# Kernel optimization log

Measured on AMD Instinct MI355X. Metric: run time of the kernel, lower is better.

## Reference

```python
import jax, jax.numpy as jnp
import numpy as np

N, E, F_IN, H, F_OUT = 50000, 400000, 128, 256, 1
EPS = 1e-5


def setup_inputs() -> dict:
    key = jax.random.key(0)
    ks = jax.random.split(key, 10)
    s = lambda fan_in: 1.0 / np.sqrt(fan_in)
    return {
        "x": jax.random.normal(ks[0], (N, F_IN), dtype=jnp.float32),
        "edge_index": jax.random.randint(ks[1], (2, E), 0, N, dtype=jnp.int64),
        # gcn1: GCNConv(F_IN -> H) + BatchNorm1d(H) params
        "W1": jax.random.uniform(ks[2], (F_IN, H), jnp.float32, -s(F_IN), s(F_IN)),
        "b1": jnp.zeros((H,), jnp.float32),
        "gamma": jnp.ones((H,), jnp.float32),
        "beta": jnp.zeros((H,), jnp.float32),
        # gcn2: GCNConv(H -> H)
        "W2": jax.random.uniform(ks[3], (H, H), jnp.float32, -s(H), s(H)),
        "b2": jnp.zeros((H,), jnp.float32),
        # ClassifierMLP2(2H -> F_OUT): Linear(2H, H) -> ReLU -> Linear(H, F_OUT)
        "Wm1": jax.random.uniform(ks[4], (2 * H, H), jnp.float32, -s(2 * H), s(2 * H)),
        "bm1": jnp.zeros((H,), jnp.float32),
        "Wm2": jax.random.uniform(ks[5], (H, F_OUT), jnp.float32, -s(H), s(H)),
        "bm2": jnp.zeros((F_OUT,), jnp.float32),
    }


def _gcn_conv(x, W, b, src_full, dst_full, norm):
    # x' = D^{-1/2} (A + I) D^{-1/2} X W + b   (self loops already appended)
    xw = x @ W                                  # [N, H]
    msg = xw[src_full] * norm[:, None]          # [E+N, H] gather + scale
    agg = jax.ops.segment_sum(msg, dst_full, num_segments=N)  # scatter-add
    return agg + b


def reference(x, edge_index, W1, b1, gamma, beta, W2, b2, Wm1, bm1, Wm2, bm2):
    src, dst = edge_index[0], edge_index[1]
    loop = jnp.arange(N, dtype=edge_index.dtype)
    src_full = jnp.concatenate([src, loop])     # add_self_loops
    dst_full = jnp.concatenate([dst, loop])
    deg = jax.ops.segment_sum(jnp.ones_like(dst_full, dtype=x.dtype), dst_full,
                              num_segments=N)   # degree of A + I (>= 1)
    dinv = jax.lax.rsqrt(deg)
    norm = dinv[src_full] * dinv[dst_full]      # [E+N] symmetric norm

    # gcn1: conv -> batchnorm (batch stats) -> relu
    h = _gcn_conv(x, W1, b1, src_full, dst_full, norm)
    mu = jnp.mean(h, axis=0)
    var = jnp.mean(jnp.square(h - mu), axis=0)  # biased var, as in BN forward
    h = (h - mu) * jax.lax.rsqrt(var + EPS) * gamma + beta
    h = jax.nn.relu(h)

    # gcn2: conv -> relu
    h = jax.nn.relu(_gcn_conv(h, W2, b2, src_full, dst_full, norm))

    # mix_node_features 'cat': per-edge concat of endpoint features
    edges_x = jnp.concatenate([h[src], h[dst]], axis=-1)  # [E, 2H]

    # ClassifierMLP2 + sigmoid
    out = jax.nn.relu(edges_x @ Wm1 + bm1) @ Wm2 + bm2
    return jax.nn.sigmoid(out)                  # [E, 1]
```

## Files before the change

### kernel.cpp

```cpp
#include <hip/hip_runtime.h>
#include <math.h>

#define NN 50000
#define EE 400000
#define FIN 128
#define HH 256
#define BN_EPS 1e-5f

typedef __attribute__((ext_vector_type(8))) short short8v;
typedef __attribute__((ext_vector_type(4))) short short4v;
typedef __attribute__((ext_vector_type(2))) short short2v;
typedef __attribute__((ext_vector_type(4))) float f32x4;

__device__ inline short f2bf(float x) {
    union { float f; unsigned u; } c; c.f = x;
    unsigned r = c.u + 0x7FFF + ((c.u >> 16) & 1);
    return (short)(r >> 16);
}
__device__ inline float bf2f(short b) {
    union { unsigned u; float f; } c; c.u = ((unsigned)(unsigned short)b) << 16;
    return c.f;
}


__global__ void k_count(const int* __restrict__ dst, int* __restrict__ cnt) {
    int e = blockIdx.x * 256 + threadIdx.x;
    if (e < EE) atomicAdd(&cnt[dst[e]], 1);
}

__global__ void k_dinv(const int* __restrict__ cnt, float* __restrict__ dinv) {
    int n = blockIdx.x * 256 + threadIdx.x;
    if (n < NN) dinv[n] = rsqrtf((float)(cnt[n] + 1));
}

__global__ __launch_bounds__(1024) void k_scan(const int* __restrict__ cnt,
                                               int* __restrict__ row_start,
                                               int* __restrict__ cursor) {
    __shared__ int sums[1024];
    int tid = threadIdx.x;
    const int per = (NN + 1023) / 1024;
    int beg = tid * per;
    int end = min(beg + per, NN);
    int s = 0;
    for (int i = beg; i < end; ++i) s += cnt[i];
    sums[tid] = s;
    __syncthreads();
    for (int off = 1; off < 1024; off <<= 1) {
        int v = (tid >= off) ? sums[tid - off] : 0;
        __syncthreads();
        if (tid >= off) sums[tid] += v;
        __syncthreads();
    }
    int prefix = (tid == 0) ? 0 : sums[tid - 1];
    for (int i = beg; i < end; ++i) {
        row_start[i] = prefix;
        cursor[i] = prefix;
        prefix += cnt[i];
    }
    if (tid == 0) row_start[NN] = sums[1023];
}

__global__ void k_fill(const int* __restrict__ src, const int* __restrict__ dst,
                       int* __restrict__ cursor, int* __restrict__ csr_src) {
    int e = blockIdx.x * 256 + threadIdx.x;
    if (e < EE) {
        int pos = atomicAdd(&cursor[dst[e]], 1);
        csr_src[pos] = src[e];
    }
}


__global__ void k_scaleX(const float* __restrict__ x, const float* __restrict__ dinv,
                         float* __restrict__ Xs) {
    int i4 = blockIdx.x * 256 + threadIdx.x;
    if (i4 >= NN * FIN / 4) return;
    float g = dinv[i4 >> 5];
    float4 v = reinterpret_cast<const float4*>(x)[i4];
    v.x *= g; v.y *= g; v.z *= g; v.w *= g;
    reinterpret_cast<float4*>(Xs)[i4] = v;
}

__global__ void k_wsplit(const float* __restrict__ src, short* __restrict__ hi,
                         short* __restrict__ lo, int K, int NC) {
    int i = blockIdx.x * 256 + threadIdx.x;
    if (i >= K * NC) return;
    int k = i / NC, n = i - k * NC;
    float v = src[i];
    short h = f2bf(v);
    short lw = f2bf(v - bf2f(h));
    size_t d = ((size_t)(k >> 3) * NC + n) * 8 + (k & 7);
    hi[d] = h;
    lo[d] = lw;
}

__global__ void k_wsplit_cat(const float* __restrict__ Wm1, short* __restrict__ hi,
                             short* __restrict__ lo) {
    int i = blockIdx.x * 256 + threadIdx.x;
    if (i >= 256 * 512) return;
    int k = i >> 9, c = i & 511;
    float v = (c < 256) ? Wm1[k * 256 + c] : Wm1[(256 + k) * 256 + (c - 256)];
    short h = f2bf(v);
    short lw = f2bf(v - bf2f(h));
    size_t d = ((size_t)(k >> 3) * 512 + c) * 8 + (k & 7);
    hi[d] = h;
    lo[d] = lw;
}


__global__ __launch_bounds__(256) void k_aggX(const float* __restrict__ Xs,
                                              const int* __restrict__ csr_src,
                                              const int* __restrict__ row_start,
                                              const float* __restrict__ dinv,
                                              short* __restrict__ Ghi,
                                              short* __restrict__ Glo) {
    int wave = threadIdx.x >> 6, lane = threadIdx.x & 63;
    int n = blockIdx.x * 4 + wave;
    if (n >= NN) return;
    const float2* base = reinterpret_cast<const float2*>(Xs);
    float2 v = base[(size_t)n * 64 + lane];
    int s0 = row_start[n], s1 = row_start[n + 1];
    for (int j = s0; j < s1; ++j) {
        float2 u = base[(size_t)csr_src[j] * 64 + lane];
        v.x += u.x; v.y += u.y;
    }
    float g = dinv[n];
    v.x *= g; v.y *= g;
    short2v h, lw;
    short h0 = f2bf(v.x), h1 = f2bf(v.y);
    h[0] = h0; h[1] = h1;
    lw[0] = f2bf(v.x - bf2f(h0)); lw[1] = f2bf(v.y - bf2f(h1));
    *(short2v*)(Ghi + (size_t)n * FIN + lane * 2) = h;
    *(short2v*)(Glo + (size_t)n * FIN + lane * 2) = lw;
}

__global__ __launch_bounds__(256) void k_aggH(const float* __restrict__ T,
                                              const int* __restrict__ csr_src,
                                              const int* __restrict__ row_start,
                                              const float* __restrict__ dinv,
                                              short* __restrict__ Ghi,
                                              short* __restrict__ Glo) {
    int wave = threadIdx.x >> 6, lane = threadIdx.x & 63;
    int n = blockIdx.x * 4 + wave;
    if (n >= NN) return;
    const float4* base = reinterpret_cast<const float4*>(T);
    float4 v = base[(size_t)n * 64 + lane];
    int s0 = row_start[n], s1 = row_start[n + 1];
    for (int j = s0; j < s1; ++j) {
        float4 u = base[(size_t)csr_src[j] * 64 + lane];
        v.x += u.x; v.y += u.y; v.z += u.z; v.w += u.w;
    }
    float g = dinv[n];
    float o[4] = {v.x * g, v.y * g, v.z * g, v.w * g};
    short4v h, lw;
#pragma unroll
    for (int j = 0; j < 4; ++j) {
        short hh = f2bf(o[j]);
        h[j] = hh;
        lw[j] = f2bf(o[j] - bf2f(hh));
    }
    *(short4v*)(Ghi + (size_t)n * HH + lane * 4) = h;
    *(short4v*)(Glo + (size_t)n * HH + lane * 4) = lw;
}


template<int K, int NC, int EPI>
__global__ __launch_bounds__(256, 2) void gemm_stripe(
    const short* __restrict__ Ahi, const short* __restrict__ Alo,
    const short* __restrict__ Bthi, const short* __restrict__ Btlo,
    const float* __restrict__ bias,
    float* __restrict__ OutF, short* __restrict__ OutH, short* __restrict__ OutL,
    short* __restrict__ OutA, short* __restrict__ OutB2, int M)
{
    constexpr int NKT = K / 32;
    constexpr int NSLAB = K / 8;
    constexpr int NPASS = NC / 64;
    __shared__ short lds[2 * NSLAB * 512];
    const int tid = threadIdx.x;
    const int w = tid >> 6, l = tid & 63;
    const int wr = w >> 1, wc = w & 1;
    const int m0 = blockIdx.x * 64;
    const int lhi = l >> 4, llo = l & 15;

    for (int s = w; s < 2 * NSLAB; s += 4) {
        int kg = (s < NSLAB) ? s : (s - NSLAB);
        const short* srcp = (s < NSLAB) ? Ahi : Alo;
        int row = m0 + l;
        if (row > M - 1) row = M - 1;
        short8v v = *(const short8v*)(srcp + (size_t)row * K + kg * 8);
        *(short8v*)(&lds[s * 512 + l * 8]) = v;
    }
    __syncthreads();

    for (int pass = 0; pass < NPASS; ++pass) {
        const int n0 = pass * 64 + wc * 32;
        f32x4 acc[2][2] = {};
#pragma unroll
        for (int kt = 0; kt < NKT; ++kt) {
            short8v bh[2], bl[2];
#pragma unroll
            for (int nt = 0; nt < 2; ++nt) {
                size_t idx = ((size_t)(kt * 4 + lhi) * NC + (n0 + nt * 16 + llo)) * 8;
                bh[nt] = *(const short8v*)(Bthi + idx);
                bl[nt] = *(const short8v*)(Btlo + idx);
            }
            short8v ah[2], al[2];
#pragma unroll
            for (int mt = 0; mt < 2; ++mt) {
                int off = (kt * 4 + lhi) * 512 + (wr * 32 + mt * 16 + llo) * 8;
                ah[mt] = *(const short8v*)(&lds[off]);
                al[mt] = *(const short8v*)(&lds[off + NSLAB * 512]);
            }
#pragma unroll
            for (int mt = 0; mt < 2; ++mt)
#pragma unroll
                for (int nt = 0; nt < 2; ++nt) {
                    acc[mt][nt] = __builtin_amdgcn_mfma_f32_16x16x32_bf16(ah[mt], bh[nt], acc[mt][nt], 0, 0, 0);
                    acc[mt][nt] = __builtin_amdgcn_mfma_f32_16x16x32_bf16(ah[mt], bl[nt], acc[mt][nt], 0, 0, 0);
                    acc[mt][nt] = __builtin_amdgcn_mfma_f32_16x16x32_bf16(al[mt], bh[nt], acc[mt][nt], 0, 0, 0);
                }
        }
#pragma unroll
        for (int mt = 0; mt < 2; ++mt)
#pragma unroll
            for (int r = 0; r < 4; ++r) {
                int gm = m0 + wr * 32 + mt * 16 + lhi * 4 + r;
                if (gm >= M) continue;
#pragma unroll
                for (int nt = 0; nt < 2; ++nt) {
                    int col = n0 + nt * 16 + llo;
                    float v = acc[mt][nt][r];
                    if constexpr (EPI == 0) {
                        OutF[(size_t)gm * NC + col] = v + bias[col];
                    } else if constexpr (EPI == 1) {
                        float o = fmaxf(v + bias[col], 0.0f);
                        short h = f2bf(o);
                        OutH[(size_t)gm * NC + col] = h;
                        OutL[(size_t)gm * NC + col] = f2bf(o - bf2f(h));
                    } else {
                        short h = f2bf(v);
                        if (col < NC / 2)
                            OutA[(size_t)gm * (NC / 2) + col] = h;
                        else
                            OutB2[(size_t)gm * (NC / 2) + col - NC / 2] = h;
                    }
                }
            }
    }
}


__global__ __launch_bounds__(256) void k_bn_stats(const float* __restrict__ Hm,
                                                  float* __restrict__ ssum,
                                                  float* __restrict__ ssq) {
    int c = threadIdx.x;
    int r0 = blockIdx.x * 64;
    int r1 = min(r0 + 64, NN);
    float s = 0.f, q = 0.f;
    for (int r = r0; r < r1; ++r) {
        float v = Hm[(size_t)r * HH + c];
        s += v;
        q += v * v;
    }
    atomicAdd(&ssum[c], s);
    atomicAdd(&ssq[c], q);
}

__global__ void k_bn_final(const float* __restrict__ ssum, const float* __restrict__ ssq,
                           const float* __restrict__ gamma, const float* __restrict__ beta,
                           float* __restrict__ scale, float* __restrict__ shift) {
    int c = threadIdx.x;
    float mu = ssum[c] / (float)NN;
    float var = ssq[c] / (float)NN - mu * mu;
    float rstd = rsqrtf(var + BN_EPS);
    float sc = rstd * gamma[c];
    scale[c] = sc;
    shift[c] = beta[c] - mu * sc;
}

__global__ void k_bn_apply_T(const float* __restrict__ P1, const float* __restrict__ scale,
                             const float* __restrict__ shift, const float* __restrict__ dinv,
                             float* __restrict__ T) {
    int i4 = blockIdx.x * 256 + threadIdx.x;
    if (i4 >= NN * HH / 4) return;
    int c4 = i4 & 63;
    float g = dinv[i4 >> 6];
    float4 v = reinterpret_cast<const float4*>(P1)[i4];
    float4 sc = reinterpret_cast<const float4*>(scale)[c4];
    float4 sh = reinterpret_cast<const float4*>(shift)[c4];
    v.x = g * fmaxf(v.x * sc.x + sh.x, 0.f);
    v.y = g * fmaxf(v.y * sc.y + sh.y, 0.f);
    v.z = g * fmaxf(v.z * sc.z + sh.z, 0.f);
    v.w = g * fmaxf(v.w * sc.w + sh.w, 0.f);
    reinterpret_cast<float4*>(T)[i4] = v;
}


__global__ __launch_bounds__(256) void k_edge(const short* __restrict__ Aarr,
                                              const short* __restrict__ Barr,
                                              const int* __restrict__ src,
                                              const int* __restrict__ dst,
                                              const float* __restrict__ bm1,
                                              const float* __restrict__ Wm2,
                                              const float* __restrict__ bm2,
                                              float* __restrict__ out) {
    int wave = threadIdx.x >> 6;
    int lane = threadIdx.x & 63;
    int e = blockIdx.x * 4 + wave;
    if (e >= EE) return;
    int s = src[e], d = dst[e];
    short4v a = *(const short4v*)(Aarr + (size_t)s * 256 + lane * 4);
    short4v b = *(const short4v*)(Barr + (size_t)d * 256 + lane * 4);
    float4 bb = reinterpret_cast<const float4*>(bm1)[lane];
    float4 w = reinterpret_cast<const float4*>(Wm2)[lane];
    float t = fmaxf(bf2f(a[0]) + bf2f(b[0]) + bb.x, 0.f) * w.x
            + fmaxf(bf2f(a[1]) + bf2f(b[1]) + bb.y, 0.f) * w.y
            + fmaxf(bf2f(a[2]) + bf2f(b[2]) + bb.z, 0.f) * w.z
            + fmaxf(bf2f(a[3]) + bf2f(b[3]) + bb.w, 0.f) * w.w;
#pragma unroll
    for (int off = 32; off; off >>= 1) t += __shfl_xor(t, off);
    if (lane == 0) {
        float z = t + bm2[0];
        out[e] = 1.0f / (1.0f + expf(-z));
    }
}


extern "C" void kernel_launch(void* const* d_in, const int* in_sizes, int n_in,
                              void* d_out, int out_size, void* d_ws, size_t ws_size,
                              hipStream_t stream) {
    const float* x     = (const float*)d_in[0];
    const int*   ei    = (const int*)d_in[1];
    const float* W1    = (const float*)d_in[2];
    const float* b1    = (const float*)d_in[3];
    const float* gamma = (const float*)d_in[4];
    const float* beta  = (const float*)d_in[5];
    const float* W2    = (const float*)d_in[6];
    const float* b2    = (const float*)d_in[7];
    const float* Wm1   = (const float*)d_in[8];
    const float* bm1   = (const float*)d_in[9];
    const float* Wm2   = (const float*)d_in[10];
    const float* bm2   = (const float*)d_in[11];
    float* out = (float*)d_out;
    const int* src = ei;
    const int* dst = ei + EE;

    char* ws = (char*)d_ws;
    size_t off = 0;
    auto take = [&](size_t b) -> char* {
        char* p = ws + off;
        off += (b + 255) & ~(size_t)255;
        return p;
    };
    int*   deg_cnt   = (int*)take((size_t)NN * 4);
    float* dinv      = (float*)take((size_t)NN * 4);
    int*   row_start = (int*)take((size_t)(NN + 1) * 4);
    int*   cursor    = (int*)take((size_t)NN * 4);
    int*   csr_src   = (int*)take((size_t)EE * 4);
    float* ssum      = (float*)take(1024);
    float* ssq       = (float*)take(1024);
    float* scale     = (float*)take(1024);
    float* shift     = (float*)take(1024);
    short* W1thi     = (short*)take((size_t)128 * 256 * 2);
    short* W1tlo     = (short*)take((size_t)128 * 256 * 2);
    short* W2thi     = (short*)take((size_t)256 * 256 * 2);
    short* W2tlo     = (short*)take((size_t)256 * 256 * 2);
    short* Wcthi     = (short*)take((size_t)256 * 512 * 2);
    short* Wctlo     = (short*)take((size_t)256 * 512 * 2);
    const size_t SLOT = (size_t)NN * HH * 4;
    char* slotA = take(SLOT);
    char* slotB = take(SLOT);
    char* slotC = take(SLOT);

    float* Xs   = (float*)slotA;
    short* G1hi = (short*)slotB;
    short* G1lo = (short*)(slotB + 12800000);
    float* P1   = (float*)slotC;
    float* T    = (float*)slotA;
    short* G2hi = (short*)slotB;
    short* G2lo = (short*)(slotB + 25600000);
    short* H2hi = (short*)slotC;
    short* H2lo = (short*)(slotC + 25600000);
    short* Aarr = (short*)slotA;
    short* Barr = (short*)(slotA + 25600000);
    (void)ssq; (void)ws_size;

    hipMemsetAsync(deg_cnt, 0, (size_t)NN * 4, stream);
    hipMemsetAsync(ssum, 0, 2048, stream);

    k_count<<<(EE + 255) / 256, 256, 0, stream>>>(dst, deg_cnt);
    k_dinv<<<(NN + 255) / 256, 256, 0, stream>>>(deg_cnt, dinv);
    k_scan<<<1, 1024, 0, stream>>>(deg_cnt, row_start, cursor);
    k_fill<<<(EE + 255) / 256, 256, 0, stream>>>(src, dst, cursor, csr_src);
    k_wsplit<<<(128 * 256 + 255) / 256, 256, 0, stream>>>(W1, W1thi, W1tlo, 128, 256);
    k_wsplit<<<(256 * 256 + 255) / 256, 256, 0, stream>>>(W2, W2thi, W2tlo, 256, 256);
    k_wsplit_cat<<<(256 * 512 + 255) / 256, 256, 0, stream>>>(Wm1, Wcthi, Wctlo);

    const int MB = (NN + 63) / 64;
    k_scaleX<<<NN * FIN / 4 / 256, 256, 0, stream>>>(x, dinv, Xs);
    k_aggX<<<(NN + 3) / 4, 256, 0, stream>>>(Xs, csr_src, row_start, dinv, G1hi, G1lo);
    gemm_stripe<128, 256, 0><<<MB, 256, 0, stream>>>(G1hi, G1lo, W1thi, W1tlo, b1,
                                                     P1, nullptr, nullptr, nullptr, nullptr, NN);
    k_bn_stats<<<(NN + 63) / 64, 256, 0, stream>>>(P1, ssum, ssq);
    k_bn_final<<<1, 256, 0, stream>>>(ssum, ssq, gamma, beta, scale, shift);
    k_bn_apply_T<<<NN * HH / 4 / 256, 256, 0, stream>>>(P1, scale, shift, dinv, T);
    k_aggH<<<(NN + 3) / 4, 256, 0, stream>>>(T, csr_src, row_start, dinv, G2hi, G2lo);
    gemm_stripe<256, 256, 1><<<MB, 256, 0, stream>>>(G2hi, G2lo, W2thi, W2tlo, b2,
                                                     nullptr, H2hi, H2lo, nullptr, nullptr, NN);
    gemm_stripe<256, 512, 2><<<MB, 256, 0, stream>>>(H2hi, H2lo, Wcthi, Wctlo, nullptr,
                                                     nullptr, nullptr, nullptr, Aarr, Barr, NN);
    k_edge<<<(EE + 3) / 4, 256, 0, stream>>>(Aarr, Barr, src, dst, bm1, Wm2, bm2, out);
}
```

Before: 656.1 us.

## Parallelize CSR prefix scan across blocks and fold X scaling into aggregation

Replaces the single-block 1024-thread serial-chunk scan with a three-kernel multi-block scan (block sums, scan of block sums, local scan plus offset), computing dinv inside the last pass. Removes the separate k_scaleX pass by applying per-source dinv inside k_aggX while gathering neighbors. This cuts a long serial single-CU kernel and a full 25MB read/write of X, at the cost of an extra dinv gather per edge in aggregation.

```diff
diff --git a/kernel.cpp b/kernel.cpp
--- a/kernel.cpp
+++ b/kernel.cpp
@@ -6,6 +6,7 @@
 #define FIN 128
 #define HH 256
 #define BN_EPS 1e-5f
+#define NSB 196
 
 typedef __attribute__((ext_vector_type(8))) short short8v;
 typedef __attribute__((ext_vector_type(4))) short short4v;
@@ -28,36 +29,59 @@
     if (e < EE) atomicAdd(&cnt[dst[e]], 1);
 }
 
-__global__ void k_dinv(const int* __restrict__ cnt, float* __restrict__ dinv) {
-    int n = blockIdx.x * 256 + threadIdx.x;
-    if (n < NN) dinv[n] = rsqrtf((float)(cnt[n] + 1));
-}
-
-__global__ __launch_bounds__(1024) void k_scan(const int* __restrict__ cnt,
+__global__ __launch_bounds__(256) void k_scan1(const int* __restrict__ cnt,
+                                               int* __restrict__ bsum) {
+    __shared__ int ws4[4];
+    int i = blockIdx.x * 256 + threadIdx.x;
+    int s = (i < NN) ? cnt[i] : 0;
+#pragma unroll
+    for (int o = 32; o; o >>= 1) s += __shfl_down(s, o);
+    if ((threadIdx.x & 63) == 0) ws4[threadIdx.x >> 6] = s;
+    __syncthreads();
+    if (threadIdx.x == 0) bsum[blockIdx.x] = ws4[0] + ws4[1] + ws4[2] + ws4[3];
+}
+
+__global__ __launch_bounds__(256) void k_scan2(const int* __restrict__ bsum,
+                                               int* __restrict__ boff,
+                                               int* __restrict__ row_start) {
+    __shared__ int sh[256];
+    int t = threadIdx.x;
+    int v = (t < NSB) ? bsum[t] : 0;
+    sh[t] = v;
+    __syncthreads();
+    for (int o = 1; o < 256; o <<= 1) {
+        int u = (t >= o) ? sh[t - o] : 0;
+        __syncthreads();
+        sh[t] += u;
+        __syncthreads();
+    }
+    if (t < NSB) boff[t] = sh[t] - v;
+    if (t == 0) row_start[NN] = EE;
+}
+
+__global__ __launch_bounds__(256) void k_scan3(const int* __restrict__ cnt,
+                                               const int* __restrict__ boff,
                                                int* __restrict__ row_start,
-                                               int* __restrict__ cursor) {
-    __shared__ int sums[1024];
-    int tid = threadIdx.x;
-    const int per = (NN + 1023) / 1024;
-    int beg = tid * per;
-    int end = min(beg + per, NN);
-    int s = 0;
-    for (int i = beg; i < end; ++i) s += cnt[i];
-    sums[tid] = s;
+                                               int* __restrict__ cursor,
+                                               float* __restrict__ dinv) {
+    __shared__ int sh[256];
+    int t = threadIdx.x;
+    int i = blockIdx.x * 256 + t;
+    int v = (i < NN) ? cnt[i] : 0;
+    sh[t] = v;
     __syncthreads();
-    for (int off = 1; off < 1024; off <<= 1) {
-        int v = (tid >= off) ? sums[tid - off] : 0;
+    for (int o = 1; o < 256; o <<= 1) {
+        int u = (t >= o) ? sh[t - o] : 0;
         __syncthreads();
-        if (tid >= off) sums[tid] += v;
+        sh[t] += u;
         __syncthreads();
     }
-    int prefix = (tid == 0) ? 0 : sums[tid - 1];
-    for (int i = beg; i < end; ++i) {
-        row_start[i] = prefix;
-        cursor[i] = prefix;
-        prefix += cnt[i];
-    }
-    if (tid == 0) row_start[NN] = sums[1023];
+    if (i < NN) {
+        int rs = boff[blockIdx.x] + sh[t] - v;
+        row_start[i] = rs;
+        cursor[i] = rs;
+        dinv[i] = rsqrtf((float)(v + 1));
+    }
 }
 
 __global__ void k_fill(const int* __restrict__ src, const int* __restrict__ dst,
@@ -69,16 +93,6 @@
     }
 }
 
-
-__global__ void k_scaleX(const float* __restrict__ x, const float* __restrict__ dinv,
-                         float* __restrict__ Xs) {
-    int i4 = blockIdx.x * 256 + threadIdx.x;
-    if (i4 >= NN * FIN / 4) return;
-    float g = dinv[i4 >> 5];
-    float4 v = reinterpret_cast<const float4*>(x)[i4];
-    v.x *= g; v.y *= g; v.z *= g; v.w *= g;
-    reinterpret_cast<float4*>(Xs)[i4] = v;
-}
 
 __global__ void k_wsplit(const float* __restrict__ src, short* __restrict__ hi,
                          short* __restrict__ lo, int K, int NC) {
@@ -107,7 +121,7 @@
 }
 
 
-__global__ __launch_bounds__(256) void k_aggX(const float* __restrict__ Xs,
+__global__ __launch_bounds__(256) void k_aggX(const float* __restrict__ x,
                                               const int* __restrict__ csr_src,
                                               const int* __restrict__ row_start,
                                               const float* __restrict__ dinv,
@@ -116,14 +130,17 @@
     int wave = threadIdx.x >> 6, lane = threadIdx.x & 63;
     int n = blockIdx.x * 4 + wave;
     if (n >= NN) return;
-    const float2* base = reinterpret_cast<const float2*>(Xs);
+    const float2* base = reinterpret_cast<const float2*>(x);
+    float g = dinv[n];
     float2 v = base[(size_t)n * 64 + lane];
+    v.x *= g; v.y *= g;
     int s0 = row_start[n], s1 = row_start[n + 1];
     for (int j = s0; j < s1; ++j) {
-        float2 u = base[(size_t)csr_src[j] * 64 + lane];
-        v.x += u.x; v.y += u.y;
-    }
-    float g = dinv[n];
+        int sj = csr_src[j];
+        float gj = dinv[sj];
+        float2 u = base[(size_t)sj * 64 + lane];
+        v.x += gj * u.x; v.y += gj * u.y;
+    }
     v.x *= g; v.y *= g;
     short2v h, lw;
     short h0 = f2bf(v.x), h1 = f2bf(v.y);
@@ -356,6 +373,8 @@
     int*   row_start = (int*)take((size_t)(NN + 1) * 4);
     int*   cursor    = (int*)take((size_t)NN * 4);
     int*   csr_src   = (int*)take((size_t)EE * 4);
+    int*   bsum      = (int*)take((size_t)NSB * 4);
+    int*   boff      = (int*)take((size_t)NSB * 4);
     float* ssum      = (float*)take(1024);
     float* ssq       = (float*)take(1024);
     float* scale     = (float*)take(1024);
@@ -371,7 +390,6 @@
     char* slotB = take(SLOT);
     char* slotC = take(SLOT);
 
-    float* Xs   = (float*)slotA;
     short* G1hi = (short*)slotB;
     short* G1lo = (short*)(slotB + 12800000);
     float* P1   = (float*)slotC;
@@ -388,16 +406,16 @@
     hipMemsetAsync(ssum, 0, 2048, stream);
 
     k_count<<<(EE + 255) / 256, 256, 0, stream>>>(dst, deg_cnt);
-    k_dinv<<<(NN + 255) / 256, 256, 0, stream>>>(deg_cnt, dinv);
-    k_scan<<<1, 1024, 0, stream>>>(deg_cnt, row_start, cursor);
+    k_scan1<<<NSB, 256, 0, stream>>>(deg_cnt, bsum);
+    k_scan2<<<1, 256, 0, stream>>>(bsum, boff, row_start);
+    k_scan3<<<NSB, 256, 0, stream>>>(deg_cnt, boff, row_start, cursor, dinv);
     k_fill<<<(EE + 255) / 256, 256, 0, stream>>>(src, dst, cursor, csr_src);
     k_wsplit<<<(128 * 256 + 255) / 256, 256, 0, stream>>>(W1, W1thi, W1tlo, 128, 256);
     k_wsplit<<<(256 * 256 + 255) / 256, 256, 0, stream>>>(W2, W2thi, W2tlo, 256, 256);
     k_wsplit_cat<<<(256 * 512 + 255) / 256, 256, 0, stream>>>(Wm1, Wcthi, Wctlo);
 
     const int MB = (NN + 63) / 64;
-    k_scaleX<<<NN * FIN / 4 / 256, 256, 0, stream>>>(x, dinv, Xs);
-    k_aggX<<<(NN + 3) / 4, 256, 0, stream>>>(Xs, csr_src, row_start, dinv, G1hi, G1lo);
+    k_aggX<<<(NN + 3) / 4, 256, 0, stream>>>(x, csr_src, row_start, dinv, G1hi, G1lo);
     gemm_stripe<128, 256, 0><<<MB, 256, 0, stream>>>(G1hi, G1lo, W1thi, W1tlo, b1,
                                                      P1, nullptr, nullptr, nullptr, nullptr, NN);
     k_bn_stats<<<(NN + 63) / 64, 256, 0, stream>>>(P1, ssum, ssq);
```

Result: faster. 546.0 us (-16.8%).
